# Kernel optimization log

Measured on AMD Instinct MI355X. Metric: run time of the kernel, lower is better.

Reference implementation:

```python
import jax, jax.numpy as jnp
import numpy as np

B = 262144
N = 2  # half of state dim 4


def setup_inputs() -> dict:
    key = jax.random.key(0)
    ks = jax.random.split(key, 7)
    return {
        "x": jax.random.normal(ks[0], (B, 4), dtype=jnp.float32),
        "W1": jax.random.normal(ks[1], (128, 4), dtype=jnp.float32) * 0.5,
        "b1": jax.random.normal(ks[2], (128,), dtype=jnp.float32) * 0.1,
        "W2": jax.random.normal(ks[3], (128, 128), dtype=jnp.float32) * 0.09,
        "b2": jax.random.normal(ks[4], (128,), dtype=jnp.float32) * 0.1,
        "W3": jax.random.normal(ks[5], (1, 128), dtype=jnp.float32) * 0.09,
        "b3": jax.random.normal(ks[6], (1,), dtype=jnp.float32) * 0.1,
    }


def _lagrangian(xi, W1, b1, W2, b2, W3, b3):
    # per-sample scalar L(q, qdot); softmax over the single feature axis
    h = jax.nn.softmax(W1 @ xi + b1)
    h = jax.nn.softmax(W2 @ h + b2)
    return (W3 @ h + b3)[0]


def reference(x, W1, b1, W2, b2, W3, b3):
    def lag(xi):
        return _lagrangian(xi, W1, b1, W2, b2, W3, b3)

    g = jax.vmap(jax.grad(lag))(x)        # (B, 4)  = jacobian rows
    H = jax.vmap(jax.hessian(lag))(x)     # (B, 4, 4)

    tqt = x[:, N:]                        # (B, 2) velocities
    # Faithful to torch code: Bi[:n, 0] picks only dL/dx0 (broadcast over 2)
    rhs = g[:, 0:1] - jnp.einsum('bij,bj->bi', H[:, N:, :N], tqt)  # (B, 2)

    # explicit 2x2 inverse of H[q', q'] block, then matvec (matches inverse @ vec)
    a = H[:, 2, 2]; b = H[:, 2, 3]; c = H[:, 3, 2]; d = H[:, 3, 3]
    det = a * d - b * c
    tqtt0 = (d * rhs[:, 0] - b * rhs[:, 1]) / det
    tqtt1 = (-c * rhs[:, 0] + a * rhs[:, 1]) / det
    tqtt = jnp.stack([tqtt0, tqtt1], axis=1)  # (B, 2) accelerations

    return jnp.concatenate([tqt, tqtt], axis=1)  # (B, 4)
```

## Files before the change

### kernel.cpp

```cpp
#include <hip/hip_runtime.h>


#define RPW 4
#define NWAVES 16
#define NTHREADS 1024
#define NGRID 256
#define NITERS 16
#define QSTRIDE 65
#define QSIZE (64 * QSTRIDE)
#define LDS_FLOATS (4 * QSIZE + NWAVES * 2 * RPW * 128)
#define LDS_BYTES (LDS_FLOATS * 4)

__device__ __forceinline__ float rlane(float v, int l) {
    return __int_as_float(__builtin_amdgcn_readlane(__float_as_int(v), l));
}

__device__ __forceinline__ float dppred(float x) {
    x += __int_as_float(__builtin_amdgcn_update_dpp(0, __float_as_int(x), 0x111, 0xf, 0xf, true));
    x += __int_as_float(__builtin_amdgcn_update_dpp(0, __float_as_int(x), 0x112, 0xf, 0xf, true));
    x += __int_as_float(__builtin_amdgcn_update_dpp(0, __float_as_int(x), 0x114, 0xf, 0xf, true));
    x += __int_as_float(__builtin_amdgcn_update_dpp(0, __float_as_int(x), 0x118, 0xf, 0xf, true));
    x += __int_as_float(__builtin_amdgcn_update_dpp(0, __float_as_int(x), 0x142, 0xa, 0xf, true));
    x += __int_as_float(__builtin_amdgcn_update_dpp(0, __float_as_int(x), 0x143, 0xc, 0xf, true));
    return rlane(x, 63);
}


__device__ __forceinline__ void mvf(const float* __restrict__ Wq,
                                    const float* __restrict__ S, int lane,
                                    float (&za)[RPW], float (&zb)[RPW])
{
    const float* w00 = Wq + 0 * QSIZE + lane * QSTRIDE;
    const float* w01 = Wq + 1 * QSIZE + lane * QSTRIDE;
    const float* w10 = Wq + 2 * QSIZE + lane * QSTRIDE;
    const float* w11 = Wq + 3 * QSIZE + lane * QSTRIDE;
#pragma unroll 4
    for (int j = 0; j < 64; j += 4) {
        const float a0 = w00[j], a1 = w00[j+1], a2 = w00[j+2], a3 = w00[j+3];
        const float b0 = w10[j], b1 = w10[j+1], b2 = w10[j+2], b3 = w10[j+3];
#pragma unroll
        for (int r = 0; r < RPW; ++r) {
            const float4 s4 = *(const float4*)(S + r * 128 + j);
            za[r] = fmaf(a0, s4.x, za[r]); za[r] = fmaf(a1, s4.y, za[r]);
            za[r] = fmaf(a2, s4.z, za[r]); za[r] = fmaf(a3, s4.w, za[r]);
            zb[r] = fmaf(b0, s4.x, zb[r]); zb[r] = fmaf(b1, s4.y, zb[r]);
            zb[r] = fmaf(b2, s4.z, zb[r]); zb[r] = fmaf(b3, s4.w, zb[r]);
        }
    }
#pragma unroll 4
    for (int j = 0; j < 64; j += 4) {
        const float a0 = w01[j], a1 = w01[j+1], a2 = w01[j+2], a3 = w01[j+3];
        const float b0 = w11[j], b1 = w11[j+1], b2 = w11[j+2], b3 = w11[j+3];
#pragma unroll
        for (int r = 0; r < RPW; ++r) {
            const float4 s4 = *(const float4*)(S + r * 128 + 64 + j);
            za[r] = fmaf(a0, s4.x, za[r]); za[r] = fmaf(a1, s4.y, za[r]);
            za[r] = fmaf(a2, s4.z, za[r]); za[r] = fmaf(a3, s4.w, za[r]);
            zb[r] = fmaf(b0, s4.x, zb[r]); zb[r] = fmaf(b1, s4.y, zb[r]);
            zb[r] = fmaf(b2, s4.z, zb[r]); zb[r] = fmaf(b3, s4.w, zb[r]);
        }
    }
}

__device__ __forceinline__ void mvf2(const float* __restrict__ Wq,
                                     const float* __restrict__ SA,
                                     const float* __restrict__ SB, int lane,
                                     float (&zAa)[RPW], float (&zAb)[RPW],
                                     float (&zBa)[RPW], float (&zBb)[RPW])
{
    const float* w00 = Wq + 0 * QSIZE + lane * QSTRIDE;
    const float* w01 = Wq + 1 * QSIZE + lane * QSTRIDE;
    const float* w10 = Wq + 2 * QSIZE + lane * QSTRIDE;
    const float* w11 = Wq + 3 * QSIZE + lane * QSTRIDE;
#pragma unroll 4
    for (int j = 0; j < 64; j += 4) {
        const float a0 = w00[j], a1 = w00[j+1], a2 = w00[j+2], a3 = w00[j+3];
        const float b0 = w10[j], b1 = w10[j+1], b2 = w10[j+2], b3 = w10[j+3];
#pragma unroll
        for (int r = 0; r < RPW; ++r) {
            const float4 x4 = *(const float4*)(SA + r * 128 + j);
            const float4 y4 = *(const float4*)(SB + r * 128 + j);
            zAa[r] = fmaf(a0, x4.x, zAa[r]); zAa[r] = fmaf(a1, x4.y, zAa[r]);
            zAa[r] = fmaf(a2, x4.z, zAa[r]); zAa[r] = fmaf(a3, x4.w, zAa[r]);
            zAb[r] = fmaf(b0, x4.x, zAb[r]); zAb[r] = fmaf(b1, x4.y, zAb[r]);
            zAb[r] = fmaf(b2, x4.z, zAb[r]); zAb[r] = fmaf(b3, x4.w, zAb[r]);
            zBa[r] = fmaf(a0, y4.x, zBa[r]); zBa[r] = fmaf(a1, y4.y, zBa[r]);
            zBa[r] = fmaf(a2, y4.z, zBa[r]); zBa[r] = fmaf(a3, y4.w, zBa[r]);
            zBb[r] = fmaf(b0, y4.x, zBb[r]); zBb[r] = fmaf(b1, y4.y, zBb[r]);
            zBb[r] = fmaf(b2, y4.z, zBb[r]); zBb[r] = fmaf(b3, y4.w, zBb[r]);
        }
    }
#pragma unroll 4
    for (int j = 0; j < 64; j += 4) {
        const float a0 = w01[j], a1 = w01[j+1], a2 = w01[j+2], a3 = w01[j+3];
        const float b0 = w11[j], b1 = w11[j+1], b2 = w11[j+2], b3 = w11[j+3];
#pragma unroll
        for (int r = 0; r < RPW; ++r) {
            const float4 x4 = *(const float4*)(SA + r * 128 + 64 + j);
            const float4 y4 = *(const float4*)(SB + r * 128 + 64 + j);
            zAa[r] = fmaf(a0, x4.x, zAa[r]); zAa[r] = fmaf(a1, x4.y, zAa[r]);
            zAa[r] = fmaf(a2, x4.z, zAa[r]); zAa[r] = fmaf(a3, x4.w, zAa[r]);
            zAb[r] = fmaf(b0, x4.x, zAb[r]); zAb[r] = fmaf(b1, x4.y, zAb[r]);
            zAb[r] = fmaf(b2, x4.z, zAb[r]); zAb[r] = fmaf(b3, x4.w, zAb[r]);
            zBa[r] = fmaf(a0, y4.x, zBa[r]); zBa[r] = fmaf(a1, y4.y, zBa[r]);
            zBa[r] = fmaf(a2, y4.z, zBa[r]); zBa[r] = fmaf(a3, y4.w, zBa[r]);
            zBb[r] = fmaf(b0, y4.x, zBb[r]); zBb[r] = fmaf(b1, y4.y, zBb[r]);
            zBb[r] = fmaf(b2, y4.z, zBb[r]); zBb[r] = fmaf(b3, y4.w, zBb[r]);
        }
    }
}

__device__ __forceinline__ void mvt(const float* __restrict__ Wq,
                                    const float* __restrict__ S, int lane,
                                    float (&za)[RPW], float (&zb)[RPW])
{
    const float* t00 = Wq + 0 * QSIZE + lane;
    const float* t01 = Wq + 1 * QSIZE + lane;
    const float* t10 = Wq + 2 * QSIZE + lane;
    const float* t11 = Wq + 3 * QSIZE + lane;
#pragma unroll 4
    for (int i = 0; i < 64; i += 4) {
        const float a0 = t00[(i+0)*QSTRIDE], a1 = t00[(i+1)*QSTRIDE],
                    a2 = t00[(i+2)*QSTRIDE], a3 = t00[(i+3)*QSTRIDE];
        const float b0 = t01[(i+0)*QSTRIDE], b1 = t01[(i+1)*QSTRIDE],
                    b2 = t01[(i+2)*QSTRIDE], b3 = t01[(i+3)*QSTRIDE];
#pragma unroll
        for (int r = 0; r < RPW; ++r) {
            const float4 u4 = *(const float4*)(S + r * 128 + i);
            za[r] = fmaf(a0, u4.x, za[r]); za[r] = fmaf(a1, u4.y, za[r]);
            za[r] = fmaf(a2, u4.z, za[r]); za[r] = fmaf(a3, u4.w, za[r]);
            zb[r] = fmaf(b0, u4.x, zb[r]); zb[r] = fmaf(b1, u4.y, zb[r]);
            zb[r] = fmaf(b2, u4.z, zb[r]); zb[r] = fmaf(b3, u4.w, zb[r]);
        }
    }
#pragma unroll 4
    for (int i = 0; i < 64; i += 4) {
        const float a0 = t10[(i+0)*QSTRIDE], a1 = t10[(i+1)*QSTRIDE],
                    a2 = t10[(i+2)*QSTRIDE], a3 = t10[(i+3)*QSTRIDE];
        const float b0 = t11[(i+0)*QSTRIDE], b1 = t11[(i+1)*QSTRIDE],
                    b2 = t11[(i+2)*QSTRIDE], b3 = t11[(i+3)*QSTRIDE];
#pragma unroll
        for (int r = 0; r < RPW; ++r) {
            const float4 u4 = *(const float4*)(S + r * 128 + 64 + i);
            za[r] = fmaf(a0, u4.x, za[r]); za[r] = fmaf(a1, u4.y, za[r]);
            za[r] = fmaf(a2, u4.z, za[r]); za[r] = fmaf(a3, u4.w, za[r]);
            zb[r] = fmaf(b0, u4.x, zb[r]); zb[r] = fmaf(b1, u4.y, zb[r]);
            zb[r] = fmaf(b2, u4.z, zb[r]); zb[r] = fmaf(b3, u4.w, zb[r]);
        }
    }
}

__device__ __forceinline__ void mvt2(const float* __restrict__ Wq,
                                     const float* __restrict__ SA,
                                     const float* __restrict__ SB, int lane,
                                     float (&zAa)[RPW], float (&zAb)[RPW],
                                     float (&zBa)[RPW], float (&zBb)[RPW])
{
    const float* t00 = Wq + 0 * QSIZE + lane;
    const float* t01 = Wq + 1 * QSIZE + lane;
    const float* t10 = Wq + 2 * QSIZE + lane;
    const float* t11 = Wq + 3 * QSIZE + lane;
#pragma unroll 4
    for (int i = 0; i < 64; i += 4) {
        const float a0 = t00[(i+0)*QSTRIDE], a1 = t00[(i+1)*QSTRIDE],
                    a2 = t00[(i+2)*QSTRIDE], a3 = t00[(i+3)*QSTRIDE];
        const float b0 = t01[(i+0)*QSTRIDE], b1 = t01[(i+1)*QSTRIDE],
                    b2 = t01[(i+2)*QSTRIDE], b3 = t01[(i+3)*QSTRIDE];
#pragma unroll
        for (int r = 0; r < RPW; ++r) {
            const float4 x4 = *(const float4*)(SA + r * 128 + i);
            const float4 y4 = *(const float4*)(SB + r * 128 + i);
            zAa[r] = fmaf(a0, x4.x, zAa[r]); zAa[r] = fmaf(a1, x4.y, zAa[r]);
            zAa[r] = fmaf(a2, x4.z, zAa[r]); zAa[r] = fmaf(a3, x4.w, zAa[r]);
            zAb[r] = fmaf(b0, x4.x, zAb[r]); zAb[r] = fmaf(b1, x4.y, zAb[r]);
            zAb[r] = fmaf(b2, x4.z, zAb[r]); zAb[r] = fmaf(b3, x4.w, zAb[r]);
            zBa[r] = fmaf(a0, y4.x, zBa[r]); zBa[r] = fmaf(a1, y4.y, zBa[r]);
            zBa[r] = fmaf(a2, y4.z, zBa[r]); zBa[r] = fmaf(a3, y4.w, zBa[r]);
            zBb[r] = fmaf(b0, y4.x, zBb[r]); zBb[r] = fmaf(b1, y4.y, zBb[r]);
            zBb[r] = fmaf(b2, y4.z, zBb[r]); zBb[r] = fmaf(b3, y4.w, zBb[r]);
        }
    }
#pragma unroll 4
    for (int i = 0; i < 64; i += 4) {
        const float a0 = t10[(i+0)*QSTRIDE], a1 = t10[(i+1)*QSTRIDE],
                    a2 = t10[(i+2)*QSTRIDE], a3 = t10[(i+3)*QSTRIDE];
        const float b0 = t11[(i+0)*QSTRIDE], b1 = t11[(i+1)*QSTRIDE],
                    b2 = t11[(i+2)*QSTRIDE], b3 = t11[(i+3)*QSTRIDE];
#pragma unroll
        for (int r = 0; r < RPW; ++r) {
            const float4 x4 = *(const float4*)(SA + r * 128 + 64 + i);
            const float4 y4 = *(const float4*)(SB + r * 128 + 64 + i);
            zAa[r] = fmaf(a0, x4.x, zAa[r]); zAa[r] = fmaf(a1, x4.y, zAa[r]);
            zAa[r] = fmaf(a2, x4.z, zAa[r]); zAa[r] = fmaf(a3, x4.w, zAa[r]);
            zAb[r] = fmaf(b0, x4.x, zAb[r]); zAb[r] = fmaf(b1, x4.y, zAb[r]);
            zAb[r] = fmaf(b2, x4.z, zAb[r]); zAb[r] = fmaf(b3, x4.w, zAb[r]);
            zBa[r] = fmaf(a0, y4.x, zBa[r]); zBa[r] = fmaf(a1, y4.y, zBa[r]);
            zBa[r] = fmaf(a2, y4.z, zBa[r]); zBa[r] = fmaf(a3, y4.w, zBa[r]);
            zBb[r] = fmaf(b0, y4.x, zBb[r]); zBb[r] = fmaf(b1, y4.y, zBb[r]);
            zBb[r] = fmaf(b2, y4.z, zBb[r]); zBb[r] = fmaf(b3, y4.w, zBb[r]);
        }
    }
}

extern "C" __global__ __launch_bounds__(NTHREADS, 4)
void lnn_kernel(const float* __restrict__ gx, const float* __restrict__ gW1,
                const float* __restrict__ gb1, const float* __restrict__ gW2,
                const float* __restrict__ gb2, const float* __restrict__ gW3,
                float* __restrict__ gout)
{
    extern __shared__ float lds[];
    float* Wq  = lds;
    float* Sst = lds + 4 * QSIZE;

    const int tid  = threadIdx.x;
    const int lane = tid & 63;
    const int wv   = tid >> 6;

    for (int e = tid; e < 16384; e += NTHREADS) {
        const int i = e >> 7, j = e & 127;
        Wq[((i >> 6) * 2 + (j >> 6)) * QSIZE + (i & 63) * QSTRIDE + (j & 63)] = gW2[e];
    }

    const int cA = lane, cB = lane + 64;
    const float w1a0 = gW1[cA * 4 + 0], w1a1 = gW1[cA * 4 + 1],
                w1a2 = gW1[cA * 4 + 2], w1a3 = gW1[cA * 4 + 3];
    const float w1b0 = gW1[cB * 4 + 0], w1b1 = gW1[cB * 4 + 1],
                w1b2 = gW1[cB * 4 + 2], w1b3 = gW1[cB * 4 + 3];
    const float b1a = gb1[cA], b1b = gb1[cB];
    const float b2a = gb2[cA], b2b = gb2[cB];
    const float w3a = gW3[cA], w3b = gW3[cB];

    __syncthreads();

    float* Sa = Sst + wv * (2 * RPW * 128);
    float* Sb = Sa + RPW * 128;

#pragma unroll 1
    for (int it = 0; it < NITERS; ++it) {
        const int row0 = blockIdx.x * (NITERS * NWAVES * RPW) + it * (NWAVES * RPW) + wv * RPW;

        float p0[RPW], p1[RPW], q0[RPW], q1[RPW], v0[RPW], v1[RPW];
        float X2[RPW], X3[RPW];
        float sw[RPW], pv[RPW], g0[RPW];

#pragma unroll
        for (int r = 0; r < RPW; ++r) {
            const float4 xr = ((const float4*)gx)[row0 + r];
            X2[r] = xr.z; X3[r] = xr.w;
            const float z1a = fmaf(w1a0, xr.x, fmaf(w1a1, xr.y, fmaf(w1a2, xr.z, fmaf(w1a3, xr.w, b1a))));
            const float z1b = fmaf(w1b0, xr.x, fmaf(w1b1, xr.y, fmaf(w1b2, xr.z, fmaf(w1b3, xr.w, b1b))));
            const float ea = __expf(z1a), eb = __expf(z1b);
            const float rs = 1.0f / dppred(ea + eb);
            p0[r] = ea * rs; p1[r] = eb * rs;
            Sa[r * 128 + lane]      = p0[r];
            Sa[r * 128 + 64 + lane] = p1[r];
        }

        float zfa[RPW], zfb[RPW];
#pragma unroll
        for (int r = 0; r < RPW; ++r) { zfa[r] = b2a; zfb[r] = b2b; }
        mvf(Wq, Sa, lane, zfa, zfb);
#pragma unroll
        for (int r = 0; r < RPW; ++r) {
            const float ea = __expf(zfa[r]), eb = __expf(zfb[r]);
            const float rs = 1.0f / dppred(ea + eb);
            q0[r] = ea * rs; q1[r] = eb * rs;
            sw[r] = dppred(fmaf(w3a, q0[r], w3b * q1[r]));
            Sa[r * 128 + lane]      = q0[r] * (w3a - sw[r]);
            Sa[r * 128 + 64 + lane] = q1[r] * (w3b - sw[r]);
        }

#pragma unroll
        for (int r = 0; r < RPW; ++r) { zfa[r] = 0.f; zfb[r] = 0.f; }
        mvt(Wq, Sa, lane, zfa, zfb);
#pragma unroll
        for (int r = 0; r < RPW; ++r) {
            v0[r] = zfa[r]; v1[r] = zfb[r];
            pv[r] = dppred(fmaf(p0[r], v0[r], p1[r] * v1[r]));
            g0[r] = dppred(fmaf(w1a0, p0[r] * (v0[r] - pv[r]), w1b0 * (p1[r] * (v1[r] - pv[r]))));
        }

        float pd20[RPW], pd21[RPW], pd30[RPW], pd31[RPW];
#pragma unroll
        for (int r = 0; r < RPW; ++r) {
            const float pi2 = dppred(fmaf(w1a2, p0[r], w1b2 * p1[r]));
            const float pi3 = dppred(fmaf(w1a3, p0[r], w1b3 * p1[r]));
            pd20[r] = p0[r] * (w1a2 - pi2); pd21[r] = p1[r] * (w1b2 - pi2);
            pd30[r] = p0[r] * (w1a3 - pi3); pd31[r] = p1[r] * (w1b3 - pi3);
            Sa[r * 128 + lane]      = pd20[r];
            Sa[r * 128 + 64 + lane] = pd21[r];
            Sb[r * 128 + lane]      = pd30[r];
            Sb[r * 128 + 64 + lane] = pd31[r];
        }
        float z2a[RPW], z2b[RPW], z3a[RPW], z3b[RPW];
#pragma unroll
        for (int r = 0; r < RPW; ++r) { z2a[r] = 0.f; z2b[r] = 0.f; z3a[r] = 0.f; z3b[r] = 0.f; }
        mvf2(Wq, Sa, Sb, lane, z2a, z2b, z3a, z3b);

#pragma unroll
        for (int r = 0; r < RPW; ++r) {
            const float zd20 = z2a[r], zd21 = z2b[r];
            const float zd30 = z3a[r], zd31 = z3b[r];
            const float sg2 = dppred(fmaf(q0[r], zd20, q1[r] * zd21));
            const float sg3 = dppred(fmaf(q0[r], zd30, q1[r] * zd31));
            const float qd20 = q0[r] * (zd20 - sg2), qd21 = q1[r] * (zd21 - sg2);
            const float qd30 = q0[r] * (zd30 - sg3), qd31 = q1[r] * (zd31 - sg3);
            const float sd2 = dppred(fmaf(w3a, qd20, w3b * qd21));
            const float sd3 = dppred(fmaf(w3a, qd30, w3b * qd31));
            Sa[r * 128 + lane]      = fmaf(qd20, w3a - sw[r], -(q0[r] * sd2));
            Sa[r * 128 + 64 + lane] = fmaf(qd21, w3b - sw[r], -(q1[r] * sd2));
            Sb[r * 128 + lane]      = fmaf(qd30, w3a - sw[r], -(q0[r] * sd3));
            Sb[r * 128 + 64 + lane] = fmaf(qd31, w3b - sw[r], -(q1[r] * sd3));
        }
#pragma unroll
        for (int r = 0; r < RPW; ++r) { z2a[r] = 0.f; z2b[r] = 0.f; z3a[r] = 0.f; z3b[r] = 0.f; }
        mvt2(Wq, Sa, Sb, lane, z2a, z2b, z3a, z3b);

#pragma unroll
        for (int r = 0; r < RPW; ++r) {
            const float vd20 = z2a[r], vd21 = z2b[r];
            const float vd30 = z3a[r], vd31 = z3b[r];
            const float dpv2 = dppred(fmaf(pd20[r], v0[r], fmaf(pd21[r], v1[r],
                               fmaf(p0[r], vd20, p1[r] * vd21))));
            const float dpv3 = dppred(fmaf(pd30[r], v0[r], fmaf(pd31[r], v1[r],
                               fmaf(p0[r], vd30, p1[r] * vd31))));
            const float gd20 = fmaf(pd20[r], v0[r] - pv[r], p0[r] * (vd20 - dpv2));
            const float gd21 = fmaf(pd21[r], v1[r] - pv[r], p1[r] * (vd21 - dpv2));
            const float gd30 = fmaf(pd30[r], v0[r] - pv[r], p0[r] * (vd30 - dpv3));
            const float gd31 = fmaf(pd31[r], v1[r] - pv[r], p1[r] * (vd31 - dpv3));
            const float h20 = dppred(fmaf(w1a0, gd20, w1b0 * gd21));
            const float h21 = dppred(fmaf(w1a1, gd20, w1b1 * gd21));
            const float h22 = dppred(fmaf(w1a2, gd20, w1b2 * gd21));
            const float h23 = dppred(fmaf(w1a3, gd20, w1b3 * gd21));
            const float h30 = dppred(fmaf(w1a0, gd30, w1b0 * gd31));
            const float h31 = dppred(fmaf(w1a1, gd30, w1b1 * gd31));
            const float h32 = dppred(fmaf(w1a2, gd30, w1b2 * gd31));
            const float h33 = dppred(fmaf(w1a3, gd30, w1b3 * gd31));

            const double rhs0 = (double)g0[r] - ((double)h20 * (double)X2[r] + (double)h21 * (double)X3[r]);
            const double rhs1 = (double)g0[r] - ((double)h30 * (double)X2[r] + (double)h31 * (double)X3[r]);
            const double a = (double)h22, b = (double)h32, c = (double)h23, d = (double)h33;
            const double det = a * d - b * c;
            const float t0 = (float)((d * rhs0 - b * rhs1) / det);
            const float t1 = (float)((a * rhs1 - c * rhs0) / det);
            if (lane == 0) {
                ((float4*)gout)[row0 + r] = make_float4(X2[r], X3[r], t0, t1);
            }
        }
    }
}

extern "C" void kernel_launch(void* const* d_in, const int* in_sizes, int n_in,
                              void* d_out, int out_size, void* d_ws, size_t ws_size,
                              hipStream_t stream)
{
    const float* gx  = (const float*)d_in[0];
    const float* gW1 = (const float*)d_in[1];
    const float* gb1 = (const float*)d_in[2];
    const float* gW2 = (const float*)d_in[3];
    const float* gb2 = (const float*)d_in[4];
    const float* gW3 = (const float*)d_in[5];
    float* gout = (float*)d_out;

    (void)hipFuncSetAttribute((const void*)lnn_kernel,
                              hipFuncAttributeMaxDynamicSharedMemorySize, LDS_BYTES);
    lnn_kernel<<<NGRID, NTHREADS, LDS_BYTES, stream>>>(gx, gW1, gb1, gW2, gb2, gW3, gout);
}
```

Measured before the change: 1.073 ms.

## Rewrite LNN kernel on bf16 MFMA with three-way split for fp32 accuracy

Replaces the per-wave FP32 FMA matrix-vector loops with bf16 MFMA 16x16x32 tiles. W2 and the activations are split into high, mid and low bf16 parts and combined through eight MFMA passes to keep near-fp32 accuracy. W2 is stored in LDS in fragment-ready forward and transposed layouts, and each wave now handles 16 rows per iteration with block and iteration counts changed. The split costs extra MFMA work and register pressure, and could lose precision in the Hessian and 2x2 solve.

```diff
diff --git a/kernel.cpp b/kernel.cpp
--- a/kernel.cpp
+++ b/kernel.cpp
@@ -1,351 +1,324 @@
 #include <hip/hip_runtime.h>
 
 
-#define RPW 4
-#define NWAVES 16
-#define NTHREADS 1024
-#define NGRID 256
-#define NITERS 16
-#define QSTRIDE 65
-#define QSIZE (64 * QSTRIDE)
-#define LDS_FLOATS (4 * QSIZE + NWAVES * 2 * RPW * 128)
-#define LDS_BYTES (LDS_FLOATS * 4)
-
-__device__ __forceinline__ float rlane(float v, int l) {
-    return __int_as_float(__builtin_amdgcn_readlane(__float_as_int(v), l));
-}
-
-__device__ __forceinline__ float dppred(float x) {
-    x += __int_as_float(__builtin_amdgcn_update_dpp(0, __float_as_int(x), 0x111, 0xf, 0xf, true));
-    x += __int_as_float(__builtin_amdgcn_update_dpp(0, __float_as_int(x), 0x112, 0xf, 0xf, true));
-    x += __int_as_float(__builtin_amdgcn_update_dpp(0, __float_as_int(x), 0x114, 0xf, 0xf, true));
-    x += __int_as_float(__builtin_amdgcn_update_dpp(0, __float_as_int(x), 0x118, 0xf, 0xf, true));
-    x += __int_as_float(__builtin_amdgcn_update_dpp(0, __float_as_int(x), 0x142, 0xa, 0xf, true));
-    x += __int_as_float(__builtin_amdgcn_update_dpp(0, __float_as_int(x), 0x143, 0xc, 0xf, true));
-    return rlane(x, 63);
-}
-
-
-__device__ __forceinline__ void mvf(const float* __restrict__ Wq,
-                                    const float* __restrict__ S, int lane,
-                                    float (&za)[RPW], float (&zb)[RPW])
-{
-    const float* w00 = Wq + 0 * QSIZE + lane * QSTRIDE;
-    const float* w01 = Wq + 1 * QSIZE + lane * QSTRIDE;
-    const float* w10 = Wq + 2 * QSIZE + lane * QSTRIDE;
-    const float* w11 = Wq + 3 * QSIZE + lane * QSTRIDE;
-#pragma unroll 4
-    for (int j = 0; j < 64; j += 4) {
-        const float a0 = w00[j], a1 = w00[j+1], a2 = w00[j+2], a3 = w00[j+3];
-        const float b0 = w10[j], b1 = w10[j+1], b2 = w10[j+2], b3 = w10[j+3];
-#pragma unroll
-        for (int r = 0; r < RPW; ++r) {
-            const float4 s4 = *(const float4*)(S + r * 128 + j);
-            za[r] = fmaf(a0, s4.x, za[r]); za[r] = fmaf(a1, s4.y, za[r]);
-            za[r] = fmaf(a2, s4.z, za[r]); za[r] = fmaf(a3, s4.w, za[r]);
-            zb[r] = fmaf(b0, s4.x, zb[r]); zb[r] = fmaf(b1, s4.y, zb[r]);
-            zb[r] = fmaf(b2, s4.z, zb[r]); zb[r] = fmaf(b3, s4.w, zb[r]);
-        }
-    }
-#pragma unroll 4
-    for (int j = 0; j < 64; j += 4) {
-        const float a0 = w01[j], a1 = w01[j+1], a2 = w01[j+2], a3 = w01[j+3];
-        const float b0 = w11[j], b1 = w11[j+1], b2 = w11[j+2], b3 = w11[j+3];
-#pragma unroll
-        for (int r = 0; r < RPW; ++r) {
-            const float4 s4 = *(const float4*)(S + r * 128 + 64 + j);
-            za[r] = fmaf(a0, s4.x, za[r]); za[r] = fmaf(a1, s4.y, za[r]);
-            za[r] = fmaf(a2, s4.z, za[r]); za[r] = fmaf(a3, s4.w, za[r]);
-            zb[r] = fmaf(b0, s4.x, zb[r]); zb[r] = fmaf(b1, s4.y, zb[r]);
-            zb[r] = fmaf(b2, s4.z, zb[r]); zb[r] = fmaf(b3, s4.w, zb[r]);
-        }
-    }
-}
-
-__device__ __forceinline__ void mvf2(const float* __restrict__ Wq,
-                                     const float* __restrict__ SA,
-                                     const float* __restrict__ SB, int lane,
-                                     float (&zAa)[RPW], float (&zAb)[RPW],
-                                     float (&zBa)[RPW], float (&zBb)[RPW])
-{
-    const float* w00 = Wq + 0 * QSIZE + lane * QSTRIDE;
-    const float* w01 = Wq + 1 * QSIZE + lane * QSTRIDE;
-    const float* w10 = Wq + 2 * QSIZE + lane * QSTRIDE;
-    const float* w11 = Wq + 3 * QSIZE + lane * QSTRIDE;
-#pragma unroll 4
-    for (int j = 0; j < 64; j += 4) {
-        const float a0 = w00[j], a1 = w00[j+1], a2 = w00[j+2], a3 = w00[j+3];
-        const float b0 = w10[j], b1 = w10[j+1], b2 = w10[j+2], b3 = w10[j+3];
-#pragma unroll
-        for (int r = 0; r < RPW; ++r) {
-            const float4 x4 = *(const float4*)(SA + r * 128 + j);
-            const float4 y4 = *(const float4*)(SB + r * 128 + j);
-            zAa[r] = fmaf(a0, x4.x, zAa[r]); zAa[r] = fmaf(a1, x4.y, zAa[r]);
-            zAa[r] = fmaf(a2, x4.z, zAa[r]); zAa[r] = fmaf(a3, x4.w, zAa[r]);
-            zAb[r] = fmaf(b0, x4.x, zAb[r]); zAb[r] = fmaf(b1, x4.y, zAb[r]);
-            zAb[r] = fmaf(b2, x4.z, zAb[r]); zAb[r] = fmaf(b3, x4.w, zAb[r]);
-            zBa[r] = fmaf(a0, y4.x, zBa[r]); zBa[r] = fmaf(a1, y4.y, zBa[r]);
-            zBa[r] = fmaf(a2, y4.z, zBa[r]); zBa[r] = fmaf(a3, y4.w, zBa[r]);
-            zBb[r] = fmaf(b0, y4.x, zBb[r]); zBb[r] = fmaf(b1, y4.y, zBb[r]);
-            zBb[r] = fmaf(b2, y4.z, zBb[r]); zBb[r] = fmaf(b3, y4.w, zBb[r]);
-        }
-    }
-#pragma unroll 4
-    for (int j = 0; j < 64; j += 4) {
-        const float a0 = w01[j], a1 = w01[j+1], a2 = w01[j+2], a3 = w01[j+3];
-        const float b0 = w11[j], b1 = w11[j+1], b2 = w11[j+2], b3 = w11[j+3];
-#pragma unroll
-        for (int r = 0; r < RPW; ++r) {
-            const float4 x4 = *(const float4*)(SA + r * 128 + 64 + j);
-            const float4 y4 = *(const float4*)(SB + r * 128 + 64 + j);
-            zAa[r] = fmaf(a0, x4.x, zAa[r]); zAa[r] = fmaf(a1, x4.y, zAa[r]);
-            zAa[r] = fmaf(a2, x4.z, zAa[r]); zAa[r] = fmaf(a3, x4.w, zAa[r]);
-            zAb[r] = fmaf(b0, x4.x, zAb[r]); zAb[r] = fmaf(b1, x4.y, zAb[r]);
-            zAb[r] = fmaf(b2, x4.z, zAb[r]); zAb[r] = fmaf(b3, x4.w, zAb[r]);
-            zBa[r] = fmaf(a0, y4.x, zBa[r]); zBa[r] = fmaf(a1, y4.y, zBa[r]);
-            zBa[r] = fmaf(a2, y4.z, zBa[r]); zBa[r] = fmaf(a3, y4.w, zBa[r]);
-            zBb[r] = fmaf(b0, y4.x, zBb[r]); zBb[r] = fmaf(b1, y4.y, zBb[r]);
-            zBb[r] = fmaf(b2, y4.z, zBb[r]); zBb[r] = fmaf(b3, y4.w, zBb[r]);
-        }
-    }
-}
-
-__device__ __forceinline__ void mvt(const float* __restrict__ Wq,
-                                    const float* __restrict__ S, int lane,
-                                    float (&za)[RPW], float (&zb)[RPW])
-{
-    const float* t00 = Wq + 0 * QSIZE + lane;
-    const float* t01 = Wq + 1 * QSIZE + lane;
-    const float* t10 = Wq + 2 * QSIZE + lane;
-    const float* t11 = Wq + 3 * QSIZE + lane;
-#pragma unroll 4
-    for (int i = 0; i < 64; i += 4) {
-        const float a0 = t00[(i+0)*QSTRIDE], a1 = t00[(i+1)*QSTRIDE],
-                    a2 = t00[(i+2)*QSTRIDE], a3 = t00[(i+3)*QSTRIDE];
-        const float b0 = t01[(i+0)*QSTRIDE], b1 = t01[(i+1)*QSTRIDE],
-                    b2 = t01[(i+2)*QSTRIDE], b3 = t01[(i+3)*QSTRIDE];
-#pragma unroll
-        for (int r = 0; r < RPW; ++r) {
-            const float4 u4 = *(const float4*)(S + r * 128 + i);
-            za[r] = fmaf(a0, u4.x, za[r]); za[r] = fmaf(a1, u4.y, za[r]);
-            za[r] = fmaf(a2, u4.z, za[r]); za[r] = fmaf(a3, u4.w, za[r]);
-            zb[r] = fmaf(b0, u4.x, zb[r]); zb[r] = fmaf(b1, u4.y, zb[r]);
-            zb[r] = fmaf(b2, u4.z, zb[r]); zb[r] = fmaf(b3, u4.w, zb[r]);
-        }
-    }
-#pragma unroll 4
-    for (int i = 0; i < 64; i += 4) {
-        const float a0 = t10[(i+0)*QSTRIDE], a1 = t10[(i+1)*QSTRIDE],
-                    a2 = t10[(i+2)*QSTRIDE], a3 = t10[(i+3)*QSTRIDE];
-        const float b0 = t11[(i+0)*QSTRIDE], b1 = t11[(i+1)*QSTRIDE],
-                    b2 = t11[(i+2)*QSTRIDE], b3 = t11[(i+3)*QSTRIDE];
-#pragma unroll
-        for (int r = 0; r < RPW; ++r) {
-            const float4 u4 = *(const float4*)(S + r * 128 + 64 + i);
-            za[r] = fmaf(a0, u4.x, za[r]); za[r] = fmaf(a1, u4.y, za[r]);
-            za[r] = fmaf(a2, u4.z, za[r]); za[r] = fmaf(a3, u4.w, za[r]);
-            zb[r] = fmaf(b0, u4.x, zb[r]); zb[r] = fmaf(b1, u4.y, zb[r]);
-            zb[r] = fmaf(b2, u4.z, zb[r]); zb[r] = fmaf(b3, u4.w, zb[r]);
-        }
-    }
-}
-
-__device__ __forceinline__ void mvt2(const float* __restrict__ Wq,
-                                     const float* __restrict__ SA,
-                                     const float* __restrict__ SB, int lane,
-                                     float (&zAa)[RPW], float (&zAb)[RPW],
-                                     float (&zBa)[RPW], float (&zBb)[RPW])
-{
-    const float* t00 = Wq + 0 * QSIZE + lane;
-    const float* t01 = Wq + 1 * QSIZE + lane;
-    const float* t10 = Wq + 2 * QSIZE + lane;
-    const float* t11 = Wq + 3 * QSIZE + lane;
-#pragma unroll 4
-    for (int i = 0; i < 64; i += 4) {
-        const float a0 = t00[(i+0)*QSTRIDE], a1 = t00[(i+1)*QSTRIDE],
-                    a2 = t00[(i+2)*QSTRIDE], a3 = t00[(i+3)*QSTRIDE];
-        const float b0 = t01[(i+0)*QSTRIDE], b1 = t01[(i+1)*QSTRIDE],
-                    b2 = t01[(i+2)*QSTRIDE], b3 = t01[(i+3)*QSTRIDE];
-#pragma unroll
-        for (int r = 0; r < RPW; ++r) {
-            const float4 x4 = *(const float4*)(SA + r * 128 + i);
-            const float4 y4 = *(const float4*)(SB + r * 128 + i);
-            zAa[r] = fmaf(a0, x4.x, zAa[r]); zAa[r] = fmaf(a1, x4.y, zAa[r]);
-            zAa[r] = fmaf(a2, x4.z, zAa[r]); zAa[r] = fmaf(a3, x4.w, zAa[r]);
-            zAb[r] = fmaf(b0, x4.x, zAb[r]); zAb[r] = fmaf(b1, x4.y, zAb[r]);
-            zAb[r] = fmaf(b2, x4.z, zAb[r]); zAb[r] = fmaf(b3, x4.w, zAb[r]);
-            zBa[r] = fmaf(a0, y4.x, zBa[r]); zBa[r] = fmaf(a1, y4.y, zBa[r]);
-            zBa[r] = fmaf(a2, y4.z, zBa[r]); zBa[r] = fmaf(a3, y4.w, zBa[r]);
-            zBb[r] = fmaf(b0, y4.x, zBb[r]); zBb[r] = fmaf(b1, y4.y, zBb[r]);
-            zBb[r] = fmaf(b2, y4.z, zBb[r]); zBb[r] = fmaf(b3, y4.w, zBb[r]);
-        }
-    }
-#pragma unroll 4
-    for (int i = 0; i < 64; i += 4) {
-        const float a0 = t10[(i+0)*QSTRIDE], a1 = t10[(i+1)*QSTRIDE],
-                    a2 = t10[(i+2)*QSTRIDE], a3 = t10[(i+3)*QSTRIDE];
-        const float b0 = t11[(i+0)*QSTRIDE], b1 = t11[(i+1)*QSTRIDE],
-                    b2 = t11[(i+2)*QSTRIDE], b3 = t11[(i+3)*QSTRIDE];
-#pragma unroll
-        for (int r = 0; r < RPW; ++r) {
-            const float4 x4 = *(const float4*)(SA + r * 128 + 64 + i);
-            const float4 y4 = *(const float4*)(SB + r * 128 + 64 + i);
-            zAa[r] = fmaf(a0, x4.x, zAa[r]); zAa[r] = fmaf(a1, x4.y, zAa[r]);
-            zAa[r] = fmaf(a2, x4.z, zAa[r]); zAa[r] = fmaf(a3, x4.w, zAa[r]);
-            zAb[r] = fmaf(b0, x4.x, zAb[r]); zAb[r] = fmaf(b1, x4.y, zAb[r]);
-            zAb[r] = fmaf(b2, x4.z, zAb[r]); zAb[r] = fmaf(b3, x4.w, zAb[r]);
-            zBa[r] = fmaf(a0, y4.x, zBa[r]); zBa[r] = fmaf(a1, y4.y, zBa[r]);
-            zBa[r] = fmaf(a2, y4.z, zBa[r]); zBa[r] = fmaf(a3, y4.w, zBa[r]);
-            zBb[r] = fmaf(b0, y4.x, zBb[r]); zBb[r] = fmaf(b1, y4.y, zBb[r]);
-            zBb[r] = fmaf(b2, y4.z, zBb[r]); zBb[r] = fmaf(b3, y4.w, zBb[r]);
-        }
-    }
-}
-
-extern "C" __global__ __launch_bounds__(NTHREADS, 4)
+using bf16x8 = __attribute__((ext_vector_type(8))) short;
+using f32x4  = __attribute__((ext_vector_type(4))) float;
+
+#define NGRID    256
+#define NTHREADS 512
+#define NITERS   8
+#define FWDH  0
+#define FWDML 32768
+#define COLH  98304
+#define LDS_BYTES 131072
+
+__device__ __forceinline__ unsigned bf16b(float x) {
+    unsigned u = __float_as_uint(x);
+    return (u + 0x7fffu + ((u >> 16) & 1u)) >> 16;
+}
+
+__device__ __forceinline__ void sp3(float a, float b, unsigned& h, unsigned& m, unsigned& l) {
+    const unsigned ha = bf16b(a), hb = bf16b(b);
+    h = ha | (hb << 16);
+    const float ra = a - __uint_as_float(ha << 16);
+    const float rb = b - __uint_as_float(hb << 16);
+    const unsigned ma = bf16b(ra), mb = bf16b(rb);
+    m = ma | (mb << 16);
+    const float qa = ra - __uint_as_float(ma << 16);
+    const float qb = rb - __uint_as_float(mb << 16);
+    l = bf16b(qa) | (bf16b(qb) << 16);
+}
+
+__device__ __forceinline__ float red4(float x) {
+    x += __shfl_xor(x, 16, 64);
+    x += __shfl_xor(x, 32, 64);
+    return x;
+}
+
+union U8 { unsigned u[4]; bf16x8 v; };
+
+#define MM(A, B, C) (C) = __builtin_amdgcn_mfma_f32_16x16x32_bf16((A), (B), (C), 0, 0, 0)
+#define PASS8(Ah, Am, Al, Bh, Bm, Bl, C) do { \
+    MM(Ah, Bh, C); MM(Ah, Bm, C); MM(Am, Bh, C); MM(Am, Bm, C); \
+    MM(Ah, Bl, C); MM(Al, Bh, C); MM(Am, Bl, C); MM(Al, Bm, C); } while (0)
+
+#define PACKB3(arr, t, Bh, Bm, Bl) do { U8 H_ = {}, M_ = {}, L_ = {}; \
+    sp3(arr[2*(t)][0],   arr[2*(t)][1],   H_.u[0], M_.u[0], L_.u[0]); \
+    sp3(arr[2*(t)][2],   arr[2*(t)][3],   H_.u[1], M_.u[1], L_.u[1]); \
+    sp3(arr[2*(t)+1][0], arr[2*(t)+1][1], H_.u[2], M_.u[2], L_.u[2]); \
+    sp3(arr[2*(t)+1][2], arr[2*(t)+1][3], H_.u[3], M_.u[3], L_.u[3]); \
+    (Bh) = H_.v; (Bm) = M_.v; (Bl) = L_.v; } while (0)
+
+#define LOADFWD(mt, t, Ah, Am, Al) do { \
+    const int fo_ = ((mt) * 4 + (t)); \
+    (Ah) = *(const bf16x8*)(aH + fo_ * 1024); \
+    const uint4 dA_ = *(const uint4*)(mlr0 + fo_ * 2048);  \
+    const uint4 dB_ = *(const uint4*)(mlr1 + fo_ * 2048);  \
+    U8 M_ = {}, L_ = {}; \
+    M_.u[0] = (dA_.x & 0xffffu) | (dA_.y << 16); \
+    M_.u[1] = (dA_.z & 0xffffu) | (dA_.w << 16); \
+    M_.u[2] = (dB_.x & 0xffffu) | (dB_.y << 16); \
+    M_.u[3] = (dB_.z & 0xffffu) | (dB_.w << 16); \
+    L_.u[0] = (dA_.x >> 16) | (dA_.y & 0xffff0000u); \
+    L_.u[1] = (dA_.z >> 16) | (dA_.w & 0xffff0000u); \
+    L_.u[2] = (dB_.x >> 16) | (dB_.y & 0xffff0000u); \
+    L_.u[3] = (dB_.z >> 16) | (dB_.w & 0xffff0000u); \
+    (Am) = M_.v; (Al) = L_.v; } while (0)
+
+#define LOADCOL(mt, t, Ah, Am, Al) do { \
+    (Ah) = *(const bf16x8*)(cH + ((mt) * 4 + (t)) * 1024); \
+    const char* q_ = colML + ((mt) >> 1) * 2048 + (t) * 16384; \
+    const unsigned x0_ = (unsigned)(((mt) & 1) << 4); \
+    const unsigned w0_ = *(const unsigned*)(q_ +           0 + x0_); \
+    const unsigned w1_ = *(const unsigned*)(q_ +         128 + (x0_ ^ 16u)); \
+    const unsigned w2_ = *(const unsigned*)(q_ +         256 + x0_); \
+    const unsigned w3_ = *(const unsigned*)(q_ +         384 + (x0_ ^ 16u)); \
+    const unsigned w4_ = *(const unsigned*)(q_ + 8192 +    0 + x0_); \
+    const unsigned w5_ = *(const unsigned*)(q_ + 8192 +  128 + (x0_ ^ 16u)); \
+    const unsigned w6_ = *(const unsigned*)(q_ + 8192 +  256 + x0_); \
+    const unsigned w7_ = *(const unsigned*)(q_ + 8192 +  384 + (x0_ ^ 16u)); \
+    U8 M_ = {}, L_ = {}; \
+    M_.u[0] = (w0_ & 0xffffu) | (w1_ << 16); \
+    M_.u[1] = (w2_ & 0xffffu) | (w3_ << 16); \
+    M_.u[2] = (w4_ & 0xffffu) | (w5_ << 16); \
+    M_.u[3] = (w6_ & 0xffffu) | (w7_ << 16); \
+    L_.u[0] = (w0_ >> 16) | (w1_ & 0xffff0000u); \
+    L_.u[1] = (w2_ >> 16) | (w3_ & 0xffff0000u); \
+    L_.u[2] = (w4_ >> 16) | (w5_ & 0xffff0000u); \
+    L_.u[3] = (w6_ >> 16) | (w7_ & 0xffff0000u); \
+    (Am) = M_.v; (Al) = L_.v; } while (0)
+
+extern "C" __global__ __launch_bounds__(NTHREADS, 2)
 void lnn_kernel(const float* __restrict__ gx, const float* __restrict__ gW1,
                 const float* __restrict__ gb1, const float* __restrict__ gW2,
                 const float* __restrict__ gb2, const float* __restrict__ gW3,
                 float* __restrict__ gout)
 {
-    extern __shared__ float lds[];
-    float* Wq  = lds;
-    float* Sst = lds + 4 * QSIZE;
-
-    const int tid  = threadIdx.x;
-    const int lane = tid & 63;
-    const int wv   = tid >> 6;
+    extern __shared__ __align__(16) char lds[];
+    const int tid = threadIdx.x;
+
+    for (int e4 = tid; e4 < (LDS_BYTES / 4); e4 += NTHREADS)
+        ((unsigned*)lds)[e4] = 0u;
+    __syncthreads();
 
     for (int e = tid; e < 16384; e += NTHREADS) {
-        const int i = e >> 7, j = e & 127;
-        Wq[((i >> 6) * 2 + (j >> 6)) * QSIZE + (i & 63) * QSTRIDE + (j & 63)] = gW2[e];
+        const int r = e >> 7, c = e & 127;
+        const float w = gW2[e];
+        const unsigned hb = bf16b(w);
+        const float r1f = w - __uint_as_float(hb << 16);
+        const unsigned mb = bf16b(r1f);
+        const float r2f = r1f - __uint_as_float(mb << 16);
+        const unsigned lb = bf16b(r2f);
+        const int fragF = (r >> 4) * 4 + (c >> 5);
+        const int sF    = (r & 15) * 4 + ((c >> 2) & 3);
+        const int eF    = ((c >> 4) & 1) * 4 + (c & 3);
+        *(unsigned short*)(lds + FWDH + fragF * 1024 + sF * 16 + eF * 2) = (unsigned short)hb;
+        *(unsigned*)(lds + FWDML + fragF * 2048 + sF * 32
+                     + ((((eF >> 2) ^ ((sF >> 2) & 1)) << 4)) + (eF & 3) * 4)
+            = mb | (lb << 16);
+        const int fragC = (c >> 4) * 4 + (r >> 5);
+        const int sC    = (c & 15) * 4 + ((r >> 2) & 3);
+        const int eC    = ((r >> 4) & 1) * 4 + (r & 3);
+        *(unsigned short*)(lds + COLH + fragC * 1024 + sC * 16 + eC * 2) = (unsigned short)hb;
     }
-
-    const int cA = lane, cB = lane + 64;
-    const float w1a0 = gW1[cA * 4 + 0], w1a1 = gW1[cA * 4 + 1],
-                w1a2 = gW1[cA * 4 + 2], w1a3 = gW1[cA * 4 + 3];
-    const float w1b0 = gW1[cB * 4 + 0], w1b1 = gW1[cB * 4 + 1],
-                w1b2 = gW1[cB * 4 + 2], w1b3 = gW1[cB * 4 + 3];
-    const float b1a = gb1[cA], b1b = gb1[cB];
-    const float b2a = gb2[cA], b2b = gb2[cB];
-    const float w3a = gW3[cA], w3b = gW3[cB];
-
     __syncthreads();
 
-    float* Sa = Sst + wv * (2 * RPW * 128);
-    float* Sb = Sa + RPW * 128;
+    const int l  = tid & 63;
+    const int wv = tid >> 6;
+    const int n  = l & 15;
+    const int gq = l >> 4;
+    const int s  = n * 4 + gq;
+
+    const char* aH    = lds + FWDH  + s * 16;
+    const char* mlr0  = lds + FWDML + s * 32 + ((n & 1) << 4);
+    const char* mlr1  = lds + FWDML + s * 32 + (((n & 1) ^ 1) << 4);
+    const char* cH    = lds + COLH  + s * 16;
+    const char* colML = lds + FWDML + gq * 512 + ((n >> 2) & 3) * 32 + (n & 3) * 4;
+
+    const float4* gW14 = (const float4*)gW1;
 
 #pragma unroll 1
     for (int it = 0; it < NITERS; ++it) {
-        const int row0 = blockIdx.x * (NITERS * NWAVES * RPW) + it * (NWAVES * RPW) + wv * RPW;
-
-        float p0[RPW], p1[RPW], q0[RPW], q1[RPW], v0[RPW], v1[RPW];
-        float X2[RPW], X3[RPW];
-        float sw[RPW], pv[RPW], g0[RPW];
-
-#pragma unroll
-        for (int r = 0; r < RPW; ++r) {
-            const float4 xr = ((const float4*)gx)[row0 + r];
-            X2[r] = xr.z; X3[r] = xr.w;
-            const float z1a = fmaf(w1a0, xr.x, fmaf(w1a1, xr.y, fmaf(w1a2, xr.z, fmaf(w1a3, xr.w, b1a))));
-            const float z1b = fmaf(w1b0, xr.x, fmaf(w1b1, xr.y, fmaf(w1b2, xr.z, fmaf(w1b3, xr.w, b1b))));
-            const float ea = __expf(z1a), eb = __expf(z1b);
-            const float rs = 1.0f / dppred(ea + eb);
-            p0[r] = ea * rs; p1[r] = eb * rs;
-            Sa[r * 128 + lane]      = p0[r];
-            Sa[r * 128 + 64 + lane] = p1[r];
-        }
-
-        float zfa[RPW], zfb[RPW];
-#pragma unroll
-        for (int r = 0; r < RPW; ++r) { zfa[r] = b2a; zfb[r] = b2b; }
-        mvf(Wq, Sa, lane, zfa, zfb);
-#pragma unroll
-        for (int r = 0; r < RPW; ++r) {
-            const float ea = __expf(zfa[r]), eb = __expf(zfb[r]);
-            const float rs = 1.0f / dppred(ea + eb);
-            q0[r] = ea * rs; q1[r] = eb * rs;
-            sw[r] = dppred(fmaf(w3a, q0[r], w3b * q1[r]));
-            Sa[r * 128 + lane]      = q0[r] * (w3a - sw[r]);
-            Sa[r * 128 + 64 + lane] = q1[r] * (w3b - sw[r]);
-        }
-
-#pragma unroll
-        for (int r = 0; r < RPW; ++r) { zfa[r] = 0.f; zfb[r] = 0.f; }
-        mvt(Wq, Sa, lane, zfa, zfb);
-#pragma unroll
-        for (int r = 0; r < RPW; ++r) {
-            v0[r] = zfa[r]; v1[r] = zfb[r];
-            pv[r] = dppred(fmaf(p0[r], v0[r], p1[r] * v1[r]));
-            g0[r] = dppred(fmaf(w1a0, p0[r] * (v0[r] - pv[r]), w1b0 * (p1[r] * (v1[r] - pv[r]))));
-        }
-
-        float pd20[RPW], pd21[RPW], pd30[RPW], pd31[RPW];
-#pragma unroll
-        for (int r = 0; r < RPW; ++r) {
-            const float pi2 = dppred(fmaf(w1a2, p0[r], w1b2 * p1[r]));
-            const float pi3 = dppred(fmaf(w1a3, p0[r], w1b3 * p1[r]));
-            pd20[r] = p0[r] * (w1a2 - pi2); pd21[r] = p1[r] * (w1b2 - pi2);
-            pd30[r] = p0[r] * (w1a3 - pi3); pd31[r] = p1[r] * (w1b3 - pi3);
-            Sa[r * 128 + lane]      = pd20[r];
-            Sa[r * 128 + 64 + lane] = pd21[r];
-            Sb[r * 128 + lane]      = pd30[r];
-            Sb[r * 128 + 64 + lane] = pd31[r];
-        }
-        float z2a[RPW], z2b[RPW], z3a[RPW], z3b[RPW];
-#pragma unroll
-        for (int r = 0; r < RPW; ++r) { z2a[r] = 0.f; z2b[r] = 0.f; z3a[r] = 0.f; z3b[r] = 0.f; }
-        mvf2(Wq, Sa, Sb, lane, z2a, z2b, z3a, z3b);
-
-#pragma unroll
-        for (int r = 0; r < RPW; ++r) {
-            const float zd20 = z2a[r], zd21 = z2b[r];
-            const float zd30 = z3a[r], zd31 = z3b[r];
-            const float sg2 = dppred(fmaf(q0[r], zd20, q1[r] * zd21));
-            const float sg3 = dppred(fmaf(q0[r], zd30, q1[r] * zd31));
-            const float qd20 = q0[r] * (zd20 - sg2), qd21 = q1[r] * (zd21 - sg2);
-            const float qd30 = q0[r] * (zd30 - sg3), qd31 = q1[r] * (zd31 - sg3);
-            const float sd2 = dppred(fmaf(w3a, qd20, w3b * qd21));
-            const float sd3 = dppred(fmaf(w3a, qd30, w3b * qd31));
-            Sa[r * 128 + lane]      = fmaf(qd20, w3a - sw[r], -(q0[r] * sd2));
-            Sa[r * 128 + 64 + lane] = fmaf(qd21, w3b - sw[r], -(q1[r] * sd2));
-            Sb[r * 128 + lane]      = fmaf(qd30, w3a - sw[r], -(q0[r] * sd3));
-            Sb[r * 128 + 64 + lane] = fmaf(qd31, w3b - sw[r], -(q1[r] * sd3));
-        }
-#pragma unroll
-        for (int r = 0; r < RPW; ++r) { z2a[r] = 0.f; z2b[r] = 0.f; z3a[r] = 0.f; z3b[r] = 0.f; }
-        mvt2(Wq, Sa, Sb, lane, z2a, z2b, z3a, z3b);
-
-#pragma unroll
-        for (int r = 0; r < RPW; ++r) {
-            const float vd20 = z2a[r], vd21 = z2b[r];
-            const float vd30 = z3a[r], vd31 = z3b[r];
-            const float dpv2 = dppred(fmaf(pd20[r], v0[r], fmaf(pd21[r], v1[r],
-                               fmaf(p0[r], vd20, p1[r] * vd21))));
-            const float dpv3 = dppred(fmaf(pd30[r], v0[r], fmaf(pd31[r], v1[r],
-                               fmaf(p0[r], vd30, p1[r] * vd31))));
-            const float gd20 = fmaf(pd20[r], v0[r] - pv[r], p0[r] * (vd20 - dpv2));
-            const float gd21 = fmaf(pd21[r], v1[r] - pv[r], p1[r] * (vd21 - dpv2));
-            const float gd30 = fmaf(pd30[r], v0[r] - pv[r], p0[r] * (vd30 - dpv3));
-            const float gd31 = fmaf(pd31[r], v1[r] - pv[r], p1[r] * (vd31 - dpv3));
-            const float h20 = dppred(fmaf(w1a0, gd20, w1b0 * gd21));
-            const float h21 = dppred(fmaf(w1a1, gd20, w1b1 * gd21));
-            const float h22 = dppred(fmaf(w1a2, gd20, w1b2 * gd21));
-            const float h23 = dppred(fmaf(w1a3, gd20, w1b3 * gd21));
-            const float h30 = dppred(fmaf(w1a0, gd30, w1b0 * gd31));
-            const float h31 = dppred(fmaf(w1a1, gd30, w1b1 * gd31));
-            const float h32 = dppred(fmaf(w1a2, gd30, w1b2 * gd31));
-            const float h33 = dppred(fmaf(w1a3, gd30, w1b3 * gd31));
-
-            const double rhs0 = (double)g0[r] - ((double)h20 * (double)X2[r] + (double)h21 * (double)X3[r]);
-            const double rhs1 = (double)g0[r] - ((double)h30 * (double)X2[r] + (double)h31 * (double)X3[r]);
-            const double a = (double)h22, b = (double)h32, c = (double)h23, d = (double)h33;
-            const double det = a * d - b * c;
-            const float t0 = (float)((d * rhs0 - b * rhs1) / det);
-            const float t1 = (float)((a * rhs1 - c * rhs0) / det);
-            if (lane == 0) {
-                ((float4*)gout)[row0 + r] = make_float4(X2[r], X3[r], t0, t1);
-            }
+        const int grow = blockIdx.x * (NITERS * 8 * 16) + wv * (NITERS * 16) + it * 16 + n;
+        const float4 xr = ((const float4*)gx)[grow];
+
+        f32x4 p[8];
+        float se = 0.f, s2a = 0.f, s3a = 0.f;
+#pragma unroll
+        for (int mt = 0; mt < 8; ++mt) {
+#pragma unroll
+            for (int j = 0; j < 4; ++j) {
+                const int c = mt * 16 + gq * 4 + j;
+                const float4 w1 = gW14[c];
+                const float z1 = fmaf(w1.x, xr.x, fmaf(w1.y, xr.y,
+                                  fmaf(w1.z, xr.z, fmaf(w1.w, xr.w, gb1[c]))));
+                const float e1 = __expf(z1);
+                p[mt][j] = e1;
+                se += e1;
+                s2a = fmaf(e1, w1.z, s2a);
+                s3a = fmaf(e1, w1.w, s3a);
+            }
+        }
+        se = red4(se); s2a = red4(s2a); s3a = red4(s3a);
+        const float rs1 = 1.0f / se;
+        const float pi2 = s2a * rs1, pi3 = s3a * rs1;
+#pragma unroll
+        for (int mt = 0; mt < 8; ++mt)
+#pragma unroll
+            for (int j = 0; j < 4; ++j) p[mt][j] *= rs1;
+
+        f32x4 az[8] = {}, a2[8] = {}, a3[8] = {};
+#pragma unroll
+        for (int t = 0; t < 4; ++t) {
+            float d2v[8], d3v[8];
+#pragma unroll
+            for (int u = 0; u < 2; ++u)
+#pragma unroll
+                for (int j = 0; j < 4; ++j) {
+                    const int c = (2 * t + u) * 16 + gq * 4 + j;
+                    const float4 w1 = gW14[c];
+                    const float pc = p[2 * t + u][j];
+                    d2v[u * 4 + j] = pc * (w1.z - pi2);
+                    d3v[u * 4 + j] = pc * (w1.w - pi3);
+                }
+            bf16x8 Bph = {}, Bpm = {}, Bpl = {}; PACKB3(p, t, Bph, Bpm, Bpl);
+            U8 H2_ = {}, M2_ = {}, L2_ = {}, H3_ = {}, M3_ = {}, L3_ = {};
+            sp3(d2v[0], d2v[1], H2_.u[0], M2_.u[0], L2_.u[0]);
+            sp3(d2v[2], d2v[3], H2_.u[1], M2_.u[1], L2_.u[1]);
+            sp3(d2v[4], d2v[5], H2_.u[2], M2_.u[2], L2_.u[2]);
+            sp3(d2v[6], d2v[7], H2_.u[3], M2_.u[3], L2_.u[3]);
+            sp3(d3v[0], d3v[1], H3_.u[0], M3_.u[0], L3_.u[0]);
+            sp3(d3v[2], d3v[3], H3_.u[1], M3_.u[1], L3_.u[1]);
+            sp3(d3v[4], d3v[5], H3_.u[2], M3_.u[2], L3_.u[2]);
+            sp3(d3v[6], d3v[7], H3_.u[3], M3_.u[3], L3_.u[3]);
+            const bf16x8 B2h = H2_.v, B2m = M2_.v, B2l = L2_.v;
+            const bf16x8 B3h = H3_.v, B3m = M3_.v, B3l = L3_.v;
+#pragma unroll
+            for (int mt = 0; mt < 8; ++mt) {
+                bf16x8 Ah = {}, Am = {}, Al = {};
+                LOADFWD(mt, t, Ah, Am, Al);
+                PASS8(Ah, Am, Al, Bph, Bpm, Bpl, az[mt]);
+                PASS8(Ah, Am, Al, B2h, B2m, B2l, a2[mt]);
+                PASS8(Ah, Am, Al, B3h, B3m, B3l, a3[mt]);
+            }
+        }
+
+        float s2 = 0.f, sw3 = 0.f, s2d2 = 0.f, s2d3 = 0.f, sw3d2 = 0.f, sw3d3 = 0.f;
+#pragma unroll
+        for (int mt = 0; mt < 8; ++mt)
+#pragma unroll
+            for (int j = 0; j < 4; ++j) {
+                const int c = mt * 16 + gq * 4 + j;
+                const float z  = az[mt][j] + gb2[c];
+                const float e2 = __expf(z);
+                const float w3c = gW3[c];
+                az[mt][j] = e2;
+                s2 += e2;
+                sw3   = fmaf(w3c, e2, sw3);
+                s2d2  = fmaf(e2, a2[mt][j], s2d2);
+                s2d3  = fmaf(e2, a3[mt][j], s2d3);
+                sw3d2 = fmaf(w3c * e2, a2[mt][j], sw3d2);
+                sw3d3 = fmaf(w3c * e2, a3[mt][j], sw3d3);
+            }
+        s2 = red4(s2); sw3 = red4(sw3); s2d2 = red4(s2d2); s2d3 = red4(s2d3);
+        sw3d2 = red4(sw3d2); sw3d3 = red4(sw3d3);
+        const float rs2 = 1.0f / s2;
+        const float sw  = sw3 * rs2;
+        const float sg2 = s2d2 * rs2, sg3 = s2d3 * rs2;
+        const float sd2 = fmaf(-sg2, sw, sw3d2 * rs2);
+        const float sd3 = fmaf(-sg3, sw, sw3d3 * rs2);
+#pragma unroll
+        for (int mt = 0; mt < 8; ++mt)
+#pragma unroll
+            for (int j = 0; j < 4; ++j) {
+                const int c = mt * 16 + gq * 4 + j;
+                const float w3c = gW3[c];
+                const float e2 = az[mt][j];
+                const float qq = e2 * rs2;
+                const float uu = qq * (w3c - sw);
+                const float zd2c = a2[mt][j], zd3c = a3[mt][j];
+                az[mt][j] = uu;
+                a2[mt][j] = fmaf(uu, zd2c - sg2, -(sd2 * qq));
+                a3[mt][j] = fmaf(uu, zd3c - sg3, -(sd3 * qq));
+            }
+
+        f32x4 av[8] = {};
+#pragma unroll
+        for (int t = 0; t < 4; ++t) {
+            bf16x8 Buh = {}, Bum = {}, Bul = {}; PACKB3(az, t, Buh, Bum, Bul);
+#pragma unroll
+            for (int mt = 0; mt < 8; ++mt) {
+                bf16x8 Ah = {}, Am = {}, Al = {};
+                LOADCOL(mt, t, Ah, Am, Al);
+                PASS8(Ah, Am, Al, Buh, Bum, Bul, av[mt]);
+            }
+        }
+        f32x4 ad2[8] = {}, ad3[8] = {};
+#pragma unroll
+        for (int t = 0; t < 4; ++t) {
+            bf16x8 B2h = {}, B2m = {}, B2l = {}; PACKB3(a2, t, B2h, B2m, B2l);
+            bf16x8 B3h = {}, B3m = {}, B3l = {}; PACKB3(a3, t, B3h, B3m, B3l);
+#pragma unroll
+            for (int mt = 0; mt < 8; ++mt) {
+                bf16x8 Ah = {}, Am = {}, Al = {};
+                LOADCOL(mt, t, Ah, Am, Al);
+                PASS8(Ah, Am, Al, B2h, B2m, B2l, ad2[mt]);
+                PASS8(Ah, Am, Al, B3h, B3m, B3l, ad3[mt]);
+            }
+        }
+
+        f32x4 pr[8];
+        float pv = 0.f, dv2 = 0.f, dv3 = 0.f;
+#pragma unroll
+        for (int mt = 0; mt < 8; ++mt)
+#pragma unroll
+            for (int j = 0; j < 4; ++j) {
+                const int c = mt * 16 + gq * 4 + j;
+                const float4 w1 = gW14[c];
+                const float z1 = fmaf(w1.x, xr.x, fmaf(w1.y, xr.y,
+                                  fmaf(w1.z, xr.z, fmaf(w1.w, xr.w, gb1[c]))));
+                const float pc = __expf(z1) * rs1;
+                pr[mt][j] = pc;
+                const float pd2c = pc * (w1.z - pi2);
+                const float pd3c = pc * (w1.w - pi3);
+                pv  = fmaf(pc, av[mt][j], pv);
+                dv2 = fmaf(pd2c, av[mt][j], fmaf(pc, ad2[mt][j], dv2));
+                dv3 = fmaf(pd3c, av[mt][j], fmaf(pc, ad3[mt][j], dv3));
+            }
+        pv = red4(pv); dv2 = red4(dv2); dv3 = red4(dv3);
+
+        float h20 = 0.f, h21 = 0.f, h22 = 0.f, h23 = 0.f;
+        float h30 = 0.f, h31 = 0.f, h32 = 0.f, h33 = 0.f, g0a = 0.f;
+#pragma unroll
+        for (int mt = 0; mt < 8; ++mt)
+#pragma unroll
+            for (int j = 0; j < 4; ++j) {
+                const int c = mt * 16 + gq * 4 + j;
+                const float4 w1 = gW14[c];
+                const float pc = pr[mt][j];
+                const float pd2c = pc * (w1.z - pi2);
+                const float pd3c = pc * (w1.w - pi3);
+                const float vm = av[mt][j] - pv;
+                const float gd2 = fmaf(pd2c, vm, pc * (ad2[mt][j] - dv2));
+                const float gd3 = fmaf(pd3c, vm, pc * (ad3[mt][j] - dv3));
+                h20 = fmaf(w1.x, gd2, h20); h21 = fmaf(w1.y, gd2, h21);
+                h22 = fmaf(w1.z, gd2, h22); h23 = fmaf(w1.w, gd2, h23);
+                h30 = fmaf(w1.x, gd3, h30); h31 = fmaf(w1.y, gd3, h31);
+                h32 = fmaf(w1.z, gd3, h32); h33 = fmaf(w1.w, gd3, h33);
+                g0a = fmaf(w1.x, pc * vm, g0a);
+            }
+        h20 = red4(h20); h21 = red4(h21); h22 = red4(h22); h23 = red4(h23);
+        h30 = red4(h30); h31 = red4(h31); h32 = red4(h32); h33 = red4(h33);
+        g0a = red4(g0a);
+
+        const double rhs0 = (double)g0a - ((double)h20 * (double)xr.z + (double)h21 * (double)xr.w);
+        const double rhs1 = (double)g0a - ((double)h30 * (double)xr.z + (double)h31 * (double)xr.w);
+        const double a_ = (double)h22, b_ = (double)h32, c_ = (double)h23, d_ = (double)h33;
+        const double det = a_ * d_ - b_ * c_;
+        const float t0 = (float)((d_ * rhs0 - b_ * rhs1) / det);
+        const float t1 = (float)((a_ * rhs1 - c_ * rhs0) / det);
+        if (gq == 0) {
+            ((float4*)gout)[grow] = make_float4(xr.z, xr.w, t0, t1);
         }
     }
 }
```

Result: slower. 2.395 ms (+123.3%).
